# Optimization experiments

Measured on AMD Instinct MI355X. Metric: run time of the kernel, lower is better.

## Reference

```python
import jax, jax.numpy as jnp
import numpy as np

K = 16  # neighbors, incl. self


def setup_inputs() -> dict:
    key = jax.random.key(0)
    ks = jax.random.split(key, 16)
    N, C = 8192, 256  # points, channels (inter_channels == in_channels == C)
    s = 0.05
    inp = {
        'coords': jax.random.uniform(ks[0], (N, 3), dtype=jnp.float32) * 100.0,
        'feats': jax.random.normal(ks[1], (N, C), dtype=jnp.float32),
        'theta_w': jax.random.normal(ks[2], (C, C), dtype=jnp.float32) * s,
        'theta_b': jax.random.normal(ks[3], (C,), dtype=jnp.float32) * s,
        'phi_w': jax.random.normal(ks[4], (C, C), dtype=jnp.float32) * s,
        'phi_b': jax.random.normal(ks[5], (C,), dtype=jnp.float32) * s,
        'g_w': jax.random.normal(ks[6], (C, C), dtype=jnp.float32) * s,
        'g_b': jax.random.normal(ks[7], (C,), dtype=jnp.float32) * s,
        'pe1_w1': jax.random.normal(ks[8], (3, C), dtype=jnp.float32) * s,
        'pe1_b1': jax.random.normal(ks[9], (C,), dtype=jnp.float32) * s,
        'pe1_w2': jax.random.normal(ks[10], (C, C), dtype=jnp.float32) * s,
        'pe1_b2': jax.random.normal(ks[11], (C,), dtype=jnp.float32) * s,
        'W_w': jax.random.normal(ks[12], (C, C), dtype=jnp.float32) * s,
        'W_b': jax.random.normal(ks[13], (C,), dtype=jnp.float32) * s,
    }
    return inp


def reference(coords, feats, theta_w, theta_b, phi_w, phi_b, g_w, g_b,
              pe1_w1, pe1_b1, pe1_w2, pe1_b2, W_w, W_b):
    C = feats.shape[-1]
    # KNN (squared dists, includes self as nearest) == pytorch3d knn_points
    sq = jnp.sum(coords * coords, axis=-1)  # [N]
    d2 = sq[:, None] + sq[None, :] - 2.0 * (coords @ coords.T)  # [N,N]
    _, idx = jax.lax.top_k(-d2, K)  # [N,K] sorted by ascending distance

    nn_coords = coords[idx]            # [N,K,3] knn gather
    nn_feats = feats[idx]              # [N,K,C]

    theta_f = feats @ theta_w + theta_b          # [N,C]
    phi_f = nn_feats @ phi_w + phi_b             # [N,K,C]

    delta_coords = nn_coords - coords[:, None, :]  # [N,K,3]
    # pe1 MLP; NOTE: original code uses pe1 for both pe1 and pe2 (shared)
    pe = jax.nn.relu(delta_coords @ pe1_w1 + pe1_b1) @ pe1_w2 + pe1_b2  # [N,K,C]

    delta_features = (pe * (theta_f[:, None, :] - phi_f) + pe) / jnp.sqrt(jnp.float32(C))
    sim = jax.nn.softmax(delta_features, axis=1)  # softmax over K neighbors

    g_feats = nn_feats @ g_w + g_b               # [N,K,C]
    y = jnp.sum(sim * g_feats, axis=1)           # [N,C]

    # W (1x1 Minkowski conv == per-point linear) + residual
    return y @ W_w + W_b + feats
```

## Files before the change

### kernel.cpp

```cpp
#include <hip/hip_runtime.h>

typedef __bf16 bf16_t;
typedef bf16_t bf16x8 __attribute__((ext_vector_type(8)));
typedef bf16_t bf16x4 __attribute__((ext_vector_type(4)));
typedef bf16_t bf16x2 __attribute__((ext_vector_type(2)));
typedef float f32x4 __attribute__((ext_vector_type(4)));
typedef unsigned long long u64;

#define N_PTS 8192
#define C_DIM 256
#define K_NN 16

#define GRID_G    16
#define GRID_NC   (GRID_G * GRID_G * GRID_G)
#define GRID_CELL 6.25f
#define GRID_INV  0.16f

#define CAST_NBLK 2048
#define PREPW_NBLK 320
__global__ __launch_bounds__(256) void prep_kernel(
    const float* __restrict__ feats, bf16_t* __restrict__ fb,
    const float* __restrict__ w0, const float* __restrict__ w1,
    const float* __restrict__ w2, const float* __restrict__ w3,
    const float* __restrict__ w4, bf16_t* __restrict__ wt_base,
    int* __restrict__ cellCount, int* __restrict__ gcount) {
    const int b = blockIdx.x;
    const int t = threadIdx.x;

    if (b < CAST_NBLK) {
        int i = (b * 256 + t) * 4;
        float4 v = *(const float4*)(feats + i);
        bf16x4 o;
        o[0] = (bf16_t)v.x; o[1] = (bf16_t)v.y; o[2] = (bf16_t)v.z; o[3] = (bf16_t)v.w;
        *(bf16x4*)(fb + i) = o;
    } else if (b < CAST_NBLK + PREPW_NBLK) {
        int pb = b - CAST_NBLK;
        int m = pb >> 6;
        int bx = pb & 63;
        const float* src = (m == 0) ? w0 : (m == 1) ? w1 : (m == 2) ? w2 : (m == 3) ? w3 : w4;
        bf16_t* dst = wt_base + m * (C_DIM * C_DIM);
#pragma unroll
        for (int i = 0; i < 4; ++i) {
            int o = bx * 1024 + i * 256 + t;
            int tkb = o >> 9;
            int rem = o & 511;
            int lm = rem >> 5;
            int r = rem & 31;
            int k = (tkb & 7) * 32 + r;
            int n = (tkb >> 3) * 16 + lm;
            dst[o] = (bf16_t)src[k * C_DIM + n];
        }
    } else {
        int zb = b - CAST_NBLK - PREPW_NBLK;
        cellCount[zb * 256 + t] = 0;
        if (zb == 0 && t == 0) *gcount = 0;
    }
}

__global__ __launch_bounds__(256) void grid_count_kernel(const float* __restrict__ coords,
                                                         int* __restrict__ cellCount,
                                                         int* __restrict__ cid) {
    int i = blockIdx.x * 256 + threadIdx.x;
    float x = coords[3 * i + 0], y = coords[3 * i + 1], z = coords[3 * i + 2];
    int cx = (int)(x * GRID_INV); if (cx > GRID_G - 1) cx = GRID_G - 1;
    int cy = (int)(y * GRID_INV); if (cy > GRID_G - 1) cy = GRID_G - 1;
    int cz = (int)(z * GRID_INV); if (cz > GRID_G - 1) cz = GRID_G - 1;
    int c = (cx * GRID_G + cy) * GRID_G + cz;
    cid[i] = c;
    atomicAdd(&cellCount[c], 1);
}

__global__ __launch_bounds__(256) void grid_scan_kernel(const int* __restrict__ cellCount,
                                                        int* __restrict__ cellStart,
                                                        int* __restrict__ cellPtr) {
    __shared__ int part[256];
    int t = threadIdx.x;
    int base = t * 16;
    int v[16];
    int sum = 0;
#pragma unroll
    for (int i = 0; i < 16; ++i) { v[i] = cellCount[base + i]; sum += v[i]; }
    part[t] = sum;
    __syncthreads();
    for (int off = 1; off < 256; off <<= 1) {
        int x = (t >= off) ? part[t - off] : 0;
        __syncthreads();
        part[t] += x;
        __syncthreads();
    }
    int acc = part[t] - sum;
#pragma unroll
    for (int i = 0; i < 16; ++i) {
        cellStart[base + i] = acc;
        cellPtr[base + i] = acc;
        acc += v[i];
    }
    if (t == 255) cellStart[GRID_NC] = acc;
}

__global__ __launch_bounds__(256) void grid_scatter_kernel(
    const float* __restrict__ coords, const int* __restrict__ cid, int* __restrict__ cellPtr,
    float* __restrict__ sx, float* __restrict__ sy, float* __restrict__ sz,
    float* __restrict__ ssq, int* __restrict__ sidx) {
    int i = blockIdx.x * 256 + threadIdx.x;
    int c = cid[i];
    int pos = atomicAdd(&cellPtr[c], 1);
    float x = coords[3 * i + 0], y = coords[3 * i + 1], z = coords[3 * i + 2];
    sx[pos] = x; sy[pos] = y; sz[pos] = z;
    ssq[pos] = __fadd_rn(__fadd_rn(__fmul_rn(x, x), __fmul_rn(y, y)), __fmul_rn(z, z));
    sidx[pos] = i;
}

__global__ __launch_bounds__(256) void knn_grid_kernel(
    const float* __restrict__ coords, const int* __restrict__ cellStart,
    const float* __restrict__ sx, const float* __restrict__ sy,
    const float* __restrict__ sz, const float* __restrict__ ssq,
    const int* __restrict__ sidx,
    int* __restrict__ idx_out, int* __restrict__ glist, int* __restrict__ gcount) {
    const int tid = threadIdx.x;
    const int wave = tid >> 6, lane = tid & 63;
    const int q = blockIdx.x * 4 + wave;

    __shared__ int segBase[4][25];
    __shared__ int segPref[4][26];

    const float qx = coords[3 * q + 0], qy = coords[3 * q + 1], qz = coords[3 * q + 2];
    const float sqi = __fadd_rn(__fadd_rn(__fmul_rn(qx, qx), __fmul_rn(qy, qy)),
                                __fmul_rn(qz, qz));

    int cx = (int)(qx * GRID_INV); if (cx > GRID_G - 1) cx = GRID_G - 1;
    int cy = (int)(qy * GRID_INV); if (cy > GRID_G - 1) cy = GRID_G - 1;
    int cz = (int)(qz * GRID_INV); if (cz > GRID_G - 1) cz = GRID_G - 1;
    int wx0 = cx - 2; if (wx0 < 0) wx0 = 0;
    int wx1 = cx + 2; if (wx1 > GRID_G - 1) wx1 = GRID_G - 1;
    int wy0 = cy - 2; if (wy0 < 0) wy0 = 0;
    int wy1 = cy + 2; if (wy1 > GRID_G - 1) wy1 = GRID_G - 1;
    int wz0 = cz - 2; if (wz0 < 0) wz0 = 0;
    int wz1 = cz + 2; if (wz1 > GRID_G - 1) wz1 = GRID_G - 1;

    const float INF = __int_as_float(0x7f800000);
    float rc = INF;
    if (wx0 > 0)          rc = fminf(rc, qx - (float)wx0 * GRID_CELL);
    if (wx1 < GRID_G - 1) rc = fminf(rc, (float)(wx1 + 1) * GRID_CELL - qx);
    if (wy0 > 0)          rc = fminf(rc, qy - (float)wy0 * GRID_CELL);
    if (wy1 < GRID_G - 1) rc = fminf(rc, (float)(wy1 + 1) * GRID_CELL - qy);
    if (wz0 > 0)          rc = fminf(rc, qz - (float)wz0 * GRID_CELL);
    if (wz1 < GRID_G - 1) rc = fminf(rc, (float)(wz1 + 1) * GRID_CELL - qz);
    float rc2 = rc * rc * 0.9999f;

    int nx = wx1 - wx0 + 1, nyc = wy1 - wy0 + 1;
    int ns = nx * nyc;
    if (lane < ns) {
        int scx = wx0 + lane / nyc;
        int scy = wy0 + lane % nyc;
        int b = (scx * GRID_G + scy) * GRID_G;
        int s0 = cellStart[b + wz0];
        int s1 = cellStart[b + wz1 + 1];
        segBase[wave][lane] = s0;
        segPref[wave][lane] = s1 - s0;
    }
    __syncthreads();
    if (lane == 0) {
        int acc = 0;
        for (int s = 0; s < ns; ++s) { int l = segPref[wave][s]; segPref[wave][s] = acc; acc += l; }
        segPref[wave][ns] = acc;
    }
    __syncthreads();

    const int M = segPref[wave][ns];
    bool flag = (M < K_NN) || (M > 320);

    u64 k0 = ~0ull, k1 = ~0ull, k2 = ~0ull, k3 = ~0ull, k4 = ~0ull;
    {
        int s = 0;
#pragma unroll
        for (int slot = 0; slot < 5; ++slot) {
            int t = lane + slot * 64;
            if (t < M) {
                while (t >= segPref[wave][s + 1]) ++s;
                int pos = segBase[wave][s] + (t - segPref[wave][s]);
                float x = sx[pos], y = sy[pos], z = sz[pos], sj = ssq[pos];
                float dot = __fmaf_rn(z, qz, __fmaf_rn(y, qy, __fmul_rn(x, qx)));
                float d2 = __fsub_rn(__fadd_rn(sqi, sj), __fmul_rn(2.0f, dot));
                unsigned u = __float_as_uint(d2);
                u = (u & 0x80000000u) ? ~u : (u | 0x80000000u);
                u64 key = (((u64)u) << 32) | (unsigned)sidx[pos];
                if (slot == 0) k0 = key;
                else if (slot == 1) k1 = key;
                else if (slot == 2) k2 = key;
                else if (slot == 3) k3 = key;
                else k4 = key;
            }
        }
    }

    u64 lm2 = k0; int li = 0;
    if (k1 < lm2) { lm2 = k1; li = 1; }
    if (k2 < lm2) { lm2 = k2; li = 2; }
    if (k3 < lm2) { lm2 = k3; li = 3; }
    if (k4 < lm2) { lm2 = k4; li = 4; }
    int keep = 0;
    u64 last = ~0ull;
#pragma unroll 1
    for (int r = 0; r < 16; ++r) {
        u64 w = lm2;
#pragma unroll
        for (int off = 1; off < 64; off <<= 1) {
            u64 o = __shfl_xor(w, off);
            w = (o < w) ? o : w;
        }
        if (lane == r) keep = (int)(unsigned)(w & 0xffffffffull);
        last = w;
        if (lm2 == w) {
            if (li == 0) k0 = ~0ull;
            else if (li == 1) k1 = ~0ull;
            else if (li == 2) k2 = ~0ull;
            else if (li == 3) k3 = ~0ull;
            else k4 = ~0ull;
            lm2 = k0; li = 0;
            if (k1 < lm2) { lm2 = k1; li = 1; }
            if (k2 < lm2) { lm2 = k2; li = 2; }
            if (k3 < lm2) { lm2 = k3; li = 3; }
            if (k4 < lm2) { lm2 = k4; li = 4; }
        }
    }

    if (!flag) {
        unsigned ou = (unsigned)(last >> 32);
        unsigned db = (ou & 0x80000000u) ? (ou ^ 0x80000000u) : ~ou;
        float d16 = __uint_as_float(db);
        if (d16 >= rc2) flag = true;
    }
    if (flag && lane == 0) {
        int sl = atomicAdd(gcount, 1);
        glist[sl] = q;
    }
    if (lane < 16) idx_out[q * K_NN + lane] = keep;
}

__global__ __launch_bounds__(256) void knn_fallback_kernel(const float* __restrict__ coords,
                                                           const int* __restrict__ glist,
                                                           const int* __restrict__ gcount,
                                                           int* __restrict__ idx_out) {
    const int count = *gcount;
    const int n0 = blockIdx.x * 4;
    if (n0 >= count) return;

    const int tid = threadIdx.x;
    const int wave = tid >> 6, lane = tid & 63;
    __shared__ float red16[4][16];
    __shared__ u64 cand[4][256];
    __shared__ int cnt[4];
    __shared__ int qids[4];

    if (tid < 4) {
        cnt[tid] = 0;
        int slot = n0 + tid;
        qids[tid] = glist[slot < count ? slot : count - 1];
    }
    __syncthreads();

    float qx[4], qy[4], qz[4], sqi[4];
#pragma unroll
    for (int q = 0; q < 4; ++q) {
        int id = qids[q];
        qx[q] = coords[3 * id + 0];
        qy[q] = coords[3 * id + 1];
        qz[q] = coords[3 * id + 2];
        sqi[q] = __fadd_rn(__fadd_rn(__fmul_rn(qx[q], qx[q]), __fmul_rn(qy[q], qy[q])),
                           __fmul_rn(qz[q], qz[q]));
    }

    const float INF = __int_as_float(0x7f800000);
    const float* cp = coords + tid * 96;

    float lmin[4] = {INF, INF, INF, INF};
#pragma unroll
    for (int c = 0; c < 4; ++c) {
        float buf[24];
#pragma unroll
        for (int v = 0; v < 6; ++v)
            *(float4*)(buf + v * 4) = *(const float4*)(cp + c * 24 + v * 4);
#pragma unroll
        for (int p = 0; p < 8; ++p) {
            float x = buf[3 * p + 0], y = buf[3 * p + 1], z = buf[3 * p + 2];
            float sqj = __fadd_rn(__fadd_rn(__fmul_rn(x, x), __fmul_rn(y, y)),
                                  __fmul_rn(z, z));
#pragma unroll
            for (int q = 0; q < 4; ++q) {
                float dot = __fmaf_rn(z, qz[q], __fmaf_rn(y, qy[q], __fmul_rn(x, qx[q])));
                float d2 = __fsub_rn(__fadd_rn(sqi[q], sqj), __fmul_rn(2.0f, dot));
                lmin[q] = fminf(lmin[q], d2);
            }
        }
    }

#pragma unroll
    for (int q = 0; q < 4; ++q) {
        float g = lmin[q];
        g = fminf(g, __shfl_xor(g, 1));
        g = fminf(g, __shfl_xor(g, 2));
        g = fminf(g, __shfl_xor(g, 4));
        g = fminf(g, __shfl_xor(g, 8));
        if ((lane & 15) == 0) red16[q][wave * 4 + (lane >> 4)] = g;
    }
    __syncthreads();

    float tau[4];
#pragma unroll
    for (int q = 0; q < 4; ++q) {
        float t = red16[q][0];
#pragma unroll
        for (int i = 1; i < 16; ++i) t = fmaxf(t, red16[q][i]);
        tau[q] = t;
    }

#pragma unroll
    for (int c = 0; c < 4; ++c) {
        float buf[24];
#pragma unroll
        for (int v = 0; v < 6; ++v)
            *(float4*)(buf + v * 4) = *(const float4*)(cp + c * 24 + v * 4);
#pragma unroll
        for (int p = 0; p < 8; ++p) {
            float x = buf[3 * p + 0], y = buf[3 * p + 1], z = buf[3 * p + 2];
            float sqj = __fadd_rn(__fadd_rn(__fmul_rn(x, x), __fmul_rn(y, y)),
                                  __fmul_rn(z, z));
            int j = tid * 32 + c * 8 + p;
#pragma unroll
            for (int q = 0; q < 4; ++q) {
                float dot = __fmaf_rn(z, qz[q], __fmaf_rn(y, qy[q], __fmul_rn(x, qx[q])));
                float d2 = __fsub_rn(__fadd_rn(sqi[q], sqj), __fmul_rn(2.0f, dot));
                if (d2 <= tau[q]) {
                    unsigned u = __float_as_uint(d2);
                    u = (u & 0x80000000u) ? ~u : (u | 0x80000000u);
                    int slot = atomicAdd(&cnt[q], 1);
                    if (slot < 256)
                        cand[q][slot] = (((u64)u) << 32) | (unsigned)j;
                }
            }
        }
    }
    __syncthreads();

    int m = cnt[wave]; if (m > 256) m = 256;
    u64 k0 = ~0ull, k1 = ~0ull, k2 = ~0ull, k3 = ~0ull;
    if (lane < m) k0 = cand[wave][lane];
    if (lane + 64 < m) k1 = cand[wave][lane + 64];
    if (lane + 128 < m) k2 = cand[wave][lane + 128];
    if (lane + 192 < m) k3 = cand[wave][lane + 192];
    u64 lm2 = k0; int li = 0;
    if (k1 < lm2) { lm2 = k1; li = 1; }
    if (k2 < lm2) { lm2 = k2; li = 2; }
    if (k3 < lm2) { lm2 = k3; li = 3; }
    int keep = 0;
#pragma unroll 1
    for (int r = 0; r < 16; ++r) {
        u64 w = lm2;
#pragma unroll
        for (int off = 1; off < 64; off <<= 1) {
            u64 o = __shfl_xor(w, off);
            w = (o < w) ? o : w;
        }
        if (lane == r) keep = (int)(unsigned)(w & 0xffffffffull);
        if (lm2 == w) {
            if (li == 0) k0 = ~0ull;
            else if (li == 1) k1 = ~0ull;
            else if (li == 2) k2 = ~0ull;
            else k3 = ~0ull;
            lm2 = k0; li = 0;
            if (k1 < lm2) { lm2 = k1; li = 1; }
            if (k2 < lm2) { lm2 = k2; li = 2; }
            if (k3 < lm2) { lm2 = k3; li = 3; }
        }
    }
    if (lane < 16) idx_out[qids[wave] * K_NN + lane] = keep;
}

__global__ __launch_bounds__(256, 2) void proj_kernel(
    const bf16_t* __restrict__ fb, const bf16_t* __restrict__ wt_base,
    const float* __restrict__ tb, const float* __restrict__ pb, const float* __restrict__ gb,
    float* __restrict__ T, bf16_t* __restrict__ PG) {
    const int sel = blockIdx.y;
    const int half = blockIdx.z;
    const bf16_t* Wt = wt_base + sel * (C_DIM * C_DIM);
    const float* bias = (sel == 0) ? tb : (sel == 1) ? pb : gb;
    const int wave = threadIdx.x >> 6, lane = threadIdx.x & 63;
    const int q = lane >> 4, lm = lane & 15;
    const int m0 = blockIdx.x * 64;

    bf16x8 bfr[2][8];
#pragma unroll
    for (int ti = 0; ti < 2; ++ti)
#pragma unroll
        for (int kb = 0; kb < 8; ++kb)
            bfr[ti][kb] = *(const bf16x8*)(Wt + (((half * 8 + wave * 2 + ti) * 8 + kb) << 9) + lm * 32 + q * 8);

    float bv[2];
#pragma unroll
    for (int ti = 0; ti < 2; ++ti) bv[ti] = bias[(half * 8 + wave * 2 + ti) * 16 + lm];

#pragma unroll
    for (int p = 0; p < 4; ++p) {
        const bf16_t* arow = fb + (m0 + p * 16 + lm) * C_DIM + q * 8;
        f32x4 acc[2];
        acc[0] = (f32x4){0.f, 0.f, 0.f, 0.f};
        acc[1] = (f32x4){0.f, 0.f, 0.f, 0.f};
#pragma unroll
        for (int kb = 0; kb < 8; ++kb) {
            bf16x8 a = *(const bf16x8*)(arow + kb * 32);
            acc[0] = __builtin_amdgcn_mfma_f32_16x16x32_bf16(a, bfr[0][kb], acc[0], 0, 0, 0);
            acc[1] = __builtin_amdgcn_mfma_f32_16x16x32_bf16(a, bfr[1][kb], acc[1], 0, 0, 0);
        }

#pragma unroll
        for (int ti = 0; ti < 2; ++ti) {
            int c = (half * 8 + wave * 2 + ti) * 16 + lm;
#pragma unroll
            for (int r = 0; r < 4; ++r) {
                float v = acc[ti][r] + bv[ti];
                int off = (m0 + p * 16 + q * 4 + r) * C_DIM + c;
                if (sel == 0) T[off] = v;
                else if (sel == 1) PG[2 * off] = (bf16_t)v;
                else PG[2 * off + 1] = (bf16_t)v;
            }
        }
    }
}

#define HPAD 264
#define P_BLK 8
#define HROWS (P_BLK * 16)
__global__ __launch_bounds__(512, 4) void pe2_fused_kernel(
    const float* __restrict__ coords, const int* __restrict__ idx,
    const float* __restrict__ T, const bf16_t* __restrict__ PG,
    const float* __restrict__ w1, const float* __restrict__ b1, const float* __restrict__ b2,
    const bf16_t* __restrict__ Wt2, bf16_t* __restrict__ yb) {
    __shared__ __align__(16) bf16_t hbuf[2][16 * HPAD];
    __shared__ float dxyz[HROWS][3];
    __shared__ int idxl[HROWS];
    const int tid = threadIdx.x;
    const int p0 = blockIdx.x * P_BLK;
    const int wave = tid >> 6, lane = tid & 63;
    const int q = lane >> 4, lm = lane & 15;

    bf16x8 bfr[2][8];
#pragma unroll
    for (int ti = 0; ti < 2; ++ti)
#pragma unroll
        for (int kb = 0; kb < 8; ++kb)
            bfr[ti][kb] = *(const bf16x8*)(Wt2 + (((wave * 2 + ti) * 8 + kb) << 9) + lm * 32 + q * 8);
    float b2c[2];
#pragma unroll
    for (int ti = 0; ti < 2; ++ti) b2c[ti] = b2[(wave * 2 + ti) * 16 + lm];

    if (tid < HROWS) {
        int n = p0 + (tid >> 4);
        int j = idx[n * K_NN + (tid & 15)];
        idxl[tid] = j;
        dxyz[tid][0] = coords[3 * j + 0] - coords[3 * n + 0];
        dxyz[tid][1] = coords[3 * j + 1] - coords[3 * n + 1];
        dxyz[tid][2] = coords[3 * j + 2] - coords[3 * n + 2];
    }
    __syncthreads();

    const int hc = tid & 255;
    const int rh = (tid >> 8) * 8;
    const float wx = w1[hc], wy = w1[C_DIM + hc], wz = w1[2 * C_DIM + hc], bb = b1[hc];

#pragma unroll
    for (int r = 0; r < 8; ++r) {
        int row = rh + r;
        float pre = dxyz[row][0] * wx + dxyz[row][1] * wy + dxyz[row][2] * wz + bb;
        hbuf[0][row * HPAD + hc] = (bf16_t)fmaxf(pre, 0.0f);
    }
    __syncthreads();

#pragma unroll 1
    for (int lp = 0; lp < P_BLK; ++lp) {
        const int n = p0 + lp;
        const int cur = lp & 1;

        int jr[4];
#pragma unroll
        for (int r = 0; r < 4; ++r) jr[r] = idxl[lp * 16 + q * 4 + r];
        bf16x2 pg[2][4];
        float Tn[2];
#pragma unroll
        for (int ti = 0; ti < 2; ++ti) {
            int c = (wave * 2 + ti) * 16 + lm;
            Tn[ti] = T[n * C_DIM + c];
#pragma unroll
            for (int r = 0; r < 4; ++r)
                pg[ti][r] = *(const bf16x2*)(PG + 2 * (jr[r] * C_DIM + c));
        }

        if (lp + 1 < P_BLK) {
            int rb = (lp + 1) * 16;
#pragma unroll
            for (int r = 0; r < 8; ++r) {
                int row = rh + r;
                float pre = dxyz[rb + row][0] * wx + dxyz[rb + row][1] * wy
                          + dxyz[rb + row][2] * wz + bb;
                hbuf[cur ^ 1][row * HPAD + hc] = (bf16_t)fmaxf(pre, 0.0f);
            }
        }

        const bf16_t* hrow = &hbuf[cur][lm * HPAD + q * 8];
        f32x4 acc[2];
        acc[0] = (f32x4){0.f, 0.f, 0.f, 0.f};
        acc[1] = (f32x4){0.f, 0.f, 0.f, 0.f};
#pragma unroll
        for (int kb = 0; kb < 8; ++kb) {
            bf16x8 a = *(const bf16x8*)(hrow + kb * 32);
            acc[0] = __builtin_amdgcn_mfma_f32_16x16x32_bf16(a, bfr[0][kb], acc[0], 0, 0, 0);
            acc[1] = __builtin_amdgcn_mfma_f32_16x16x32_bf16(a, bfr[1][kb], acc[1], 0, 0, 0);
        }

#pragma unroll
        for (int ti = 0; ti < 2; ++ti) {
            int c = (wave * 2 + ti) * 16 + lm;
            float df[4];
#pragma unroll
            for (int r = 0; r < 4; ++r) {
                float pe = acc[ti][r] + b2c[ti];
                df[r] = (pe * (Tn[ti] - (float)pg[ti][r][0]) + pe) * 0.0625f;
            }
            float mx = fmaxf(fmaxf(df[0], df[1]), fmaxf(df[2], df[3]));
            mx = fmaxf(mx, __shfl_xor(mx, 16));
            mx = fmaxf(mx, __shfl_xor(mx, 32));
            float e[4], s = 0.f;
#pragma unroll
            for (int r = 0; r < 4; ++r) { e[r] = __expf(df[r] - mx); s += e[r]; }
            s += __shfl_xor(s, 16);
            s += __shfl_xor(s, 32);
            float inv = 1.0f / s;
            float y = 0.f;
#pragma unroll
            for (int r = 0; r < 4; ++r) y += e[r] * inv * (float)pg[ti][r][1];
            y += __shfl_xor(y, 16);
            y += __shfl_xor(y, 32);
            if (q == 0) yb[n * C_DIM + c] = (bf16_t)y;
        }
        __syncthreads();
    }
}

__global__ __launch_bounds__(256, 2) void final_kernel(
    const bf16_t* __restrict__ yb, const bf16_t* __restrict__ Wt,
    const float* __restrict__ Wb, const float* __restrict__ feats,
    float* __restrict__ out) {
    const int wave = threadIdx.x >> 6, lane = threadIdx.x & 63;
    const int q = lane >> 4, lm = lane & 15;
    const int m0 = blockIdx.x * 64;
    const int half = blockIdx.y;

    bf16x8 bfr[2][8];
#pragma unroll
    for (int ti = 0; ti < 2; ++ti)
#pragma unroll
        for (int kb = 0; kb < 8; ++kb)
            bfr[ti][kb] = *(const bf16x8*)(Wt + (((half * 8 + wave * 2 + ti) * 8 + kb) << 9) + lm * 32 + q * 8);
    float bv[2];
#pragma unroll
    for (int ti = 0; ti < 2; ++ti) bv[ti] = Wb[(half * 8 + wave * 2 + ti) * 16 + lm];

#pragma unroll
    for (int p = 0; p < 4; ++p) {
        const bf16_t* arow = yb + (m0 + p * 16 + lm) * C_DIM + q * 8;
        f32x4 acc[2];
        acc[0] = (f32x4){0.f, 0.f, 0.f, 0.f};
        acc[1] = (f32x4){0.f, 0.f, 0.f, 0.f};
#pragma unroll
        for (int kb = 0; kb < 8; ++kb) {
            bf16x8 a = *(const bf16x8*)(arow + kb * 32);
            acc[0] = __builtin_amdgcn_mfma_f32_16x16x32_bf16(a, bfr[0][kb], acc[0], 0, 0, 0);
            acc[1] = __builtin_amdgcn_mfma_f32_16x16x32_bf16(a, bfr[1][kb], acc[1], 0, 0, 0);
        }

#pragma unroll
        for (int ti = 0; ti < 2; ++ti) {
            int c = (half * 8 + wave * 2 + ti) * 16 + lm;
#pragma unroll
            for (int r = 0; r < 4; ++r) {
                int off = (m0 + p * 16 + q * 4 + r) * C_DIM + c;
                out[off] = acc[ti][r] + bv[ti] + feats[off];
            }
        }
    }
}

extern "C" void kernel_launch(void* const* d_in, const int* in_sizes, int n_in,
                              void* d_out, int out_size, void* d_ws, size_t ws_size,
                              hipStream_t stream) {
    const float* coords = (const float*)d_in[0];
    const float* feats  = (const float*)d_in[1];
    const float* theta_w = (const float*)d_in[2];
    const float* theta_b = (const float*)d_in[3];
    const float* phi_w   = (const float*)d_in[4];
    const float* phi_b   = (const float*)d_in[5];
    const float* g_w     = (const float*)d_in[6];
    const float* g_b     = (const float*)d_in[7];
    const float* pe1_w1  = (const float*)d_in[8];
    const float* pe1_b1  = (const float*)d_in[9];
    const float* pe1_w2  = (const float*)d_in[10];
    const float* pe1_b2  = (const float*)d_in[11];
    const float* W_w     = (const float*)d_in[12];
    const float* W_b     = (const float*)d_in[13];
    float* out = (float*)d_out;

    char* w = (char*)d_ws;
    size_t off = 0;
    int* idx = (int*)(w + off);        off += (size_t)N_PTS * K_NN * 4;
    bf16_t* fb = (bf16_t*)(w + off);   off += (size_t)N_PTS * C_DIM * 2;
    bf16_t* wt = (bf16_t*)(w + off);   off += (size_t)5 * C_DIM * C_DIM * 2;
    float* T = (float*)(w + off);      off += (size_t)N_PTS * C_DIM * 4;
    bf16_t* PG = (bf16_t*)(w + off);   off += (size_t)N_PTS * C_DIM * 4;
    bf16_t* yb = (bf16_t*)(w + off);   off += (size_t)N_PTS * C_DIM * 2;
    int* cid       = (int*)(w + off);  off += (size_t)N_PTS * 4;
    int* cellCount = (int*)(w + off);  off += (size_t)GRID_NC * 4;
    int* cellStart = (int*)(w + off);  off += (size_t)(GRID_NC + 1) * 4;
    int* cellPtr   = (int*)(w + off);  off += (size_t)GRID_NC * 4;
    float* sxp = (float*)(w + off);    off += (size_t)N_PTS * 4;
    float* syp = (float*)(w + off);    off += (size_t)N_PTS * 4;
    float* szp = (float*)(w + off);    off += (size_t)N_PTS * 4;
    float* ssqp = (float*)(w + off);   off += (size_t)N_PTS * 4;
    int* sidxp = (int*)(w + off);      off += (size_t)N_PTS * 4;
    int* glist = (int*)(w + off);      off += (size_t)N_PTS * 4;
    int* gcount = (int*)(w + off);     off += 256;
    (void)ws_size; (void)in_sizes; (void)n_in; (void)out_size;

    prep_kernel<<<CAST_NBLK + PREPW_NBLK + 16, 256, 0, stream>>>(
        feats, fb, theta_w, phi_w, g_w, pe1_w2, W_w, wt, cellCount, gcount);

    grid_count_kernel<<<N_PTS / 256, 256, 0, stream>>>(coords, cellCount, cid);
    grid_scan_kernel<<<1, 256, 0, stream>>>(cellCount, cellStart, cellPtr);
    grid_scatter_kernel<<<N_PTS / 256, 256, 0, stream>>>(coords, cid, cellPtr,
                                                         sxp, syp, szp, ssqp, sidxp);
    knn_grid_kernel<<<N_PTS / 4, 256, 0, stream>>>(coords, cellStart, sxp, syp, szp,
                                                   ssqp, sidxp, idx, glist, gcount);
    knn_fallback_kernel<<<N_PTS / 4, 256, 0, stream>>>(coords, glist, gcount, idx);

    proj_kernel<<<dim3(N_PTS / 64, 3, 2), 256, 0, stream>>>(fb, wt, theta_b, phi_b, g_b, T, PG);
    pe2_fused_kernel<<<N_PTS / P_BLK, 512, 0, stream>>>(coords, idx, T, PG,
                                                        pe1_w1, pe1_b1, pe1_b2,
                                                        wt + 3 * C_DIM * C_DIM, yb);
    final_kernel<<<dim3(N_PTS / 64, 2), 256, 0, stream>>>(yb, wt + 4 * C_DIM * C_DIM,
                                                          W_b, feats, out);
}
```

Baseline: 197.9 us.

## Pack sorted coords as float4, grid-stride KNN fallback, enlarge pe2 point block

New measurement: 195.5 us. About the same (-1.2%).

```diff
diff --git a/kernel.cpp b/kernel.cpp
--- a/kernel.cpp
+++ b/kernel.cpp
@@ -100,22 +100,19 @@
 
 __global__ __launch_bounds__(256) void grid_scatter_kernel(
     const float* __restrict__ coords, const int* __restrict__ cid, int* __restrict__ cellPtr,
-    float* __restrict__ sx, float* __restrict__ sy, float* __restrict__ sz,
-    float* __restrict__ ssq, int* __restrict__ sidx) {
+    float4* __restrict__ sp4, int* __restrict__ sidx) {
     int i = blockIdx.x * 256 + threadIdx.x;
     int c = cid[i];
     int pos = atomicAdd(&cellPtr[c], 1);
     float x = coords[3 * i + 0], y = coords[3 * i + 1], z = coords[3 * i + 2];
-    sx[pos] = x; sy[pos] = y; sz[pos] = z;
-    ssq[pos] = __fadd_rn(__fadd_rn(__fmul_rn(x, x), __fmul_rn(y, y)), __fmul_rn(z, z));
+    float sq = __fadd_rn(__fadd_rn(__fmul_rn(x, x), __fmul_rn(y, y)), __fmul_rn(z, z));
+    sp4[pos] = make_float4(x, y, z, sq);
     sidx[pos] = i;
 }
 
 __global__ __launch_bounds__(256) void knn_grid_kernel(
     const float* __restrict__ coords, const int* __restrict__ cellStart,
-    const float* __restrict__ sx, const float* __restrict__ sy,
-    const float* __restrict__ sz, const float* __restrict__ ssq,
-    const int* __restrict__ sidx,
+    const float4* __restrict__ sp4, const int* __restrict__ sidx,
     int* __restrict__ idx_out, int* __restrict__ glist, int* __restrict__ gcount) {
     const int tid = threadIdx.x;
     const int wave = tid >> 6, lane = tid & 63;
@@ -179,9 +176,9 @@
             if (t < M) {
                 while (t >= segPref[wave][s + 1]) ++s;
                 int pos = segBase[wave][s] + (t - segPref[wave][s]);
-                float x = sx[pos], y = sy[pos], z = sz[pos], sj = ssq[pos];
-                float dot = __fmaf_rn(z, qz, __fmaf_rn(y, qy, __fmul_rn(x, qx)));
-                float d2 = __fsub_rn(__fadd_rn(sqi, sj), __fmul_rn(2.0f, dot));
+                float4 v = sp4[pos];
+                float dot = __fmaf_rn(v.z, qz, __fmaf_rn(v.y, qy, __fmul_rn(v.x, qx)));
+                float d2 = __fsub_rn(__fadd_rn(sqi, v.w), __fmul_rn(2.0f, dot));
                 unsigned u = __float_as_uint(d2);
                 u = (u & 0x80000000u) ? ~u : (u | 0x80000000u);
                 u64 key = (((u64)u) << 32) | (unsigned)sidx[pos];
@@ -243,138 +240,139 @@
                                                            const int* __restrict__ gcount,
                                                            int* __restrict__ idx_out) {
     const int count = *gcount;
-    const int n0 = blockIdx.x * 4;
-    if (n0 >= count) return;
-
     const int tid = threadIdx.x;
     const int wave = tid >> 6, lane = tid & 63;
     __shared__ float red16[4][16];
     __shared__ u64 cand[4][256];
     __shared__ int cnt[4];
     __shared__ int qids[4];
-
-    if (tid < 4) {
-        cnt[tid] = 0;
-        int slot = n0 + tid;
-        qids[tid] = glist[slot < count ? slot : count - 1];
-    }
-    __syncthreads();
-
-    float qx[4], qy[4], qz[4], sqi[4];
-#pragma unroll
-    for (int q = 0; q < 4; ++q) {
-        int id = qids[q];
-        qx[q] = coords[3 * id + 0];
-        qy[q] = coords[3 * id + 1];
-        qz[q] = coords[3 * id + 2];
-        sqi[q] = __fadd_rn(__fadd_rn(__fmul_rn(qx[q], qx[q]), __fmul_rn(qy[q], qy[q])),
-                           __fmul_rn(qz[q], qz[q]));
-    }
-
     const float INF = __int_as_float(0x7f800000);
     const float* cp = coords + tid * 96;
 
-    float lmin[4] = {INF, INF, INF, INF};
-#pragma unroll
-    for (int c = 0; c < 4; ++c) {
-        float buf[24];
-#pragma unroll
-        for (int v = 0; v < 6; ++v)
-            *(float4*)(buf + v * 4) = *(const float4*)(cp + c * 24 + v * 4);
-#pragma unroll
-        for (int p = 0; p < 8; ++p) {
-            float x = buf[3 * p + 0], y = buf[3 * p + 1], z = buf[3 * p + 2];
-            float sqj = __fadd_rn(__fadd_rn(__fmul_rn(x, x), __fmul_rn(y, y)),
-                                  __fmul_rn(z, z));
-#pragma unroll
-            for (int q = 0; q < 4; ++q) {
-                float dot = __fmaf_rn(z, qz[q], __fmaf_rn(y, qy[q], __fmul_rn(x, qx[q])));
-                float d2 = __fsub_rn(__fadd_rn(sqi[q], sqj), __fmul_rn(2.0f, dot));
-                lmin[q] = fminf(lmin[q], d2);
-            }
-        }
-    }
-
-#pragma unroll
-    for (int q = 0; q < 4; ++q) {
-        float g = lmin[q];
-        g = fminf(g, __shfl_xor(g, 1));
-        g = fminf(g, __shfl_xor(g, 2));
-        g = fminf(g, __shfl_xor(g, 4));
-        g = fminf(g, __shfl_xor(g, 8));
-        if ((lane & 15) == 0) red16[q][wave * 4 + (lane >> 4)] = g;
-    }
-    __syncthreads();
-
-    float tau[4];
-#pragma unroll
-    for (int q = 0; q < 4; ++q) {
-        float t = red16[q][0];
-#pragma unroll
-        for (int i = 1; i < 16; ++i) t = fmaxf(t, red16[q][i]);
-        tau[q] = t;
-    }
-
-#pragma unroll
-    for (int c = 0; c < 4; ++c) {
-        float buf[24];
-#pragma unroll
-        for (int v = 0; v < 6; ++v)
-            *(float4*)(buf + v * 4) = *(const float4*)(cp + c * 24 + v * 4);
-#pragma unroll
-        for (int p = 0; p < 8; ++p) {
-            float x = buf[3 * p + 0], y = buf[3 * p + 1], z = buf[3 * p + 2];
-            float sqj = __fadd_rn(__fadd_rn(__fmul_rn(x, x), __fmul_rn(y, y)),
-                                  __fmul_rn(z, z));
-            int j = tid * 32 + c * 8 + p;
-#pragma unroll
-            for (int q = 0; q < 4; ++q) {
-                float dot = __fmaf_rn(z, qz[q], __fmaf_rn(y, qy[q], __fmul_rn(x, qx[q])));
-                float d2 = __fsub_rn(__fadd_rn(sqi[q], sqj), __fmul_rn(2.0f, dot));
-                if (d2 <= tau[q]) {
-                    unsigned u = __float_as_uint(d2);
-                    u = (u & 0x80000000u) ? ~u : (u | 0x80000000u);
-                    int slot = atomicAdd(&cnt[q], 1);
-                    if (slot < 256)
-                        cand[q][slot] = (((u64)u) << 32) | (unsigned)j;
+#pragma unroll 1
+    for (int n0 = blockIdx.x * 4; n0 < count; n0 += gridDim.x * 4) {
+        if (tid < 4) {
+            cnt[tid] = 0;
+            int slot = n0 + tid;
+            qids[tid] = glist[slot < count ? slot : count - 1];
+        }
+        __syncthreads();
+
+        float qx[4], qy[4], qz[4], sqi[4];
+#pragma unroll
+        for (int q = 0; q < 4; ++q) {
+            int id = qids[q];
+            qx[q] = coords[3 * id + 0];
+            qy[q] = coords[3 * id + 1];
+            qz[q] = coords[3 * id + 2];
+            sqi[q] = __fadd_rn(__fadd_rn(__fmul_rn(qx[q], qx[q]), __fmul_rn(qy[q], qy[q])),
+                               __fmul_rn(qz[q], qz[q]));
+        }
+
+        float lmin[4] = {INF, INF, INF, INF};
+#pragma unroll
+        for (int c = 0; c < 4; ++c) {
+            float buf[24];
+#pragma unroll
+            for (int v = 0; v < 6; ++v)
+                *(float4*)(buf + v * 4) = *(const float4*)(cp + c * 24 + v * 4);
+#pragma unroll
+            for (int p = 0; p < 8; ++p) {
+                float x = buf[3 * p + 0], y = buf[3 * p + 1], z = buf[3 * p + 2];
+                float sqj = __fadd_rn(__fadd_rn(__fmul_rn(x, x), __fmul_rn(y, y)),
+                                      __fmul_rn(z, z));
+#pragma unroll
+                for (int q = 0; q < 4; ++q) {
+                    float dot = __fmaf_rn(z, qz[q], __fmaf_rn(y, qy[q], __fmul_rn(x, qx[q])));
+                    float d2 = __fsub_rn(__fadd_rn(sqi[q], sqj), __fmul_rn(2.0f, dot));
+                    lmin[q] = fminf(lmin[q], d2);
                 }
             }
         }
-    }
-    __syncthreads();
-
-    int m = cnt[wave]; if (m > 256) m = 256;
-    u64 k0 = ~0ull, k1 = ~0ull, k2 = ~0ull, k3 = ~0ull;
-    if (lane < m) k0 = cand[wave][lane];
-    if (lane + 64 < m) k1 = cand[wave][lane + 64];
-    if (lane + 128 < m) k2 = cand[wave][lane + 128];
-    if (lane + 192 < m) k3 = cand[wave][lane + 192];
-    u64 lm2 = k0; int li = 0;
-    if (k1 < lm2) { lm2 = k1; li = 1; }
-    if (k2 < lm2) { lm2 = k2; li = 2; }
-    if (k3 < lm2) { lm2 = k3; li = 3; }
-    int keep = 0;
+
+#pragma unroll
+        for (int q = 0; q < 4; ++q) {
+            float g = lmin[q];
+            g = fminf(g, __shfl_xor(g, 1));
+            g = fminf(g, __shfl_xor(g, 2));
+            g = fminf(g, __shfl_xor(g, 4));
+            g = fminf(g, __shfl_xor(g, 8));
+            if ((lane & 15) == 0) red16[q][wave * 4 + (lane >> 4)] = g;
+        }
+        __syncthreads();
+
+        float tau[4];
+#pragma unroll
+        for (int q = 0; q < 4; ++q) {
+            float t = red16[q][0];
+#pragma unroll
+            for (int i = 1; i < 16; ++i) t = fmaxf(t, red16[q][i]);
+            tau[q] = t;
+        }
+
+#pragma unroll
+        for (int c = 0; c < 4; ++c) {
+            float buf[24];
+#pragma unroll
+            for (int v = 0; v < 6; ++v)
+                *(float4*)(buf + v * 4) = *(const float4*)(cp + c * 24 + v * 4);
+#pragma unroll
+            for (int p = 0; p < 8; ++p) {
+                float x = buf[3 * p + 0], y = buf[3 * p + 1], z = buf[3 * p + 2];
+                float sqj = __fadd_rn(__fadd_rn(__fmul_rn(x, x), __fmul_rn(y, y)),
+                                      __fmul_rn(z, z));
+                int j = tid * 32 + c * 8 + p;
+#pragma unroll
+                for (int q = 0; q < 4; ++q) {
+                    float dot = __fmaf_rn(z, qz[q], __fmaf_rn(y, qy[q], __fmul_rn(x, qx[q])));
+                    float d2 = __fsub_rn(__fadd_rn(sqi[q], sqj), __fmul_rn(2.0f, dot));
+                    if (d2 <= tau[q]) {
+                        unsigned u = __float_as_uint(d2);
+                        u = (u & 0x80000000u) ? ~u : (u | 0x80000000u);
+                        int slot = atomicAdd(&cnt[q], 1);
+                        if (slot < 256)
+                            cand[q][slot] = (((u64)u) << 32) | (unsigned)j;
+                    }
+                }
+            }
+        }
+        __syncthreads();
+
+        int m = cnt[wave]; if (m > 256) m = 256;
+        u64 k0 = ~0ull, k1 = ~0ull, k2 = ~0ull, k3 = ~0ull;
+        if (lane < m) k0 = cand[wave][lane];
+        if (lane + 64 < m) k1 = cand[wave][lane + 64];
+        if (lane + 128 < m) k2 = cand[wave][lane + 128];
+        if (lane + 192 < m) k3 = cand[wave][lane + 192];
+        u64 lm2 = k0; int li = 0;
+        if (k1 < lm2) { lm2 = k1; li = 1; }
+        if (k2 < lm2) { lm2 = k2; li = 2; }
+        if (k3 < lm2) { lm2 = k3; li = 3; }
+        int keep = 0;
 #pragma unroll 1
-    for (int r = 0; r < 16; ++r) {
-        u64 w = lm2;
-#pragma unroll
-        for (int off = 1; off < 64; off <<= 1) {
-            u64 o = __shfl_xor(w, off);
-            w = (o < w) ? o : w;
-        }
-        if (lane == r) keep = (int)(unsigned)(w & 0xffffffffull);
-        if (lm2 == w) {
-            if (li == 0) k0 = ~0ull;
-            else if (li == 1) k1 = ~0ull;
-            else if (li == 2) k2 = ~0ull;
-            else k3 = ~0ull;
-            lm2 = k0; li = 0;
-            if (k1 < lm2) { lm2 = k1; li = 1; }
-            if (k2 < lm2) { lm2 = k2; li = 2; }
-            if (k3 < lm2) { lm2 = k3; li = 3; }
-        }
-    }
-    if (lane < 16) idx_out[qids[wave] * K_NN + lane] = keep;
+        for (int r = 0; r < 16; ++r) {
+            u64 w = lm2;
+#pragma unroll
+            for (int off = 1; off < 64; off <<= 1) {
+                u64 o = __shfl_xor(w, off);
+                w = (o < w) ? o : w;
+            }
+            if (lane == r) keep = (int)(unsigned)(w & 0xffffffffull);
+            if (lm2 == w) {
+                if (li == 0) k0 = ~0ull;
+                else if (li == 1) k1 = ~0ull;
+                else if (li == 2) k2 = ~0ull;
+                else k3 = ~0ull;
+                lm2 = k0; li = 0;
+                if (k1 < lm2) { lm2 = k1; li = 1; }
+                if (k2 < lm2) { lm2 = k2; li = 2; }
+                if (k3 < lm2) { lm2 = k3; li = 3; }
+            }
+        }
+        if (n0 + wave < count && lane < 16)
+            idx_out[qids[wave] * K_NN + lane] = keep;
+        __syncthreads();
+    }
 }
 
 __global__ __launch_bounds__(256, 2) void proj_kernel(
@@ -429,7 +427,7 @@
 }
 
 #define HPAD 264
-#define P_BLK 8
+#define P_BLK 16
 #define HROWS (P_BLK * 16)
 __global__ __launch_bounds__(512, 4) void pe2_fused_kernel(
     const float* __restrict__ coords, const int* __restrict__ idx,
@@ -617,15 +615,12 @@
     float* T = (float*)(w + off);      off += (size_t)N_PTS * C_DIM * 4;
     bf16_t* PG = (bf16_t*)(w + off);   off += (size_t)N_PTS * C_DIM * 4;
     bf16_t* yb = (bf16_t*)(w + off);   off += (size_t)N_PTS * C_DIM * 2;
+    float4* sp4 = (float4*)(w + off);  off += (size_t)N_PTS * 16;
+    int* sidxp = (int*)(w + off);      off += (size_t)N_PTS * 4;
     int* cid       = (int*)(w + off);  off += (size_t)N_PTS * 4;
     int* cellCount = (int*)(w + off);  off += (size_t)GRID_NC * 4;
     int* cellStart = (int*)(w + off);  off += (size_t)(GRID_NC + 1) * 4;
     int* cellPtr   = (int*)(w + off);  off += (size_t)GRID_NC * 4;
-    float* sxp = (float*)(w + off);    off += (size_t)N_PTS * 4;
-    float* syp = (float*)(w + off);    off += (size_t)N_PTS * 4;
-    float* szp = (float*)(w + off);    off += (size_t)N_PTS * 4;
-    float* ssqp = (float*)(w + off);   off += (size_t)N_PTS * 4;
-    int* sidxp = (int*)(w + off);      off += (size_t)N_PTS * 4;
     int* glist = (int*)(w + off);      off += (size_t)N_PTS * 4;
     int* gcount = (int*)(w + off);     off += 256;
     (void)ws_size; (void)in_sizes; (void)n_in; (void)out_size;
@@ -635,11 +630,10 @@
 
     grid_count_kernel<<<N_PTS / 256, 256, 0, stream>>>(coords, cellCount, cid);
     grid_scan_kernel<<<1, 256, 0, stream>>>(cellCount, cellStart, cellPtr);
-    grid_scatter_kernel<<<N_PTS / 256, 256, 0, stream>>>(coords, cid, cellPtr,
-                                                         sxp, syp, szp, ssqp, sidxp);
-    knn_grid_kernel<<<N_PTS / 4, 256, 0, stream>>>(coords, cellStart, sxp, syp, szp,
-                                                   ssqp, sidxp, idx, glist, gcount);
-    knn_fallback_kernel<<<N_PTS / 4, 256, 0, stream>>>(coords, glist, gcount, idx);
+    grid_scatter_kernel<<<N_PTS / 256, 256, 0, stream>>>(coords, cid, cellPtr, sp4, sidxp);
+    knn_grid_kernel<<<N_PTS / 4, 256, 0, stream>>>(coords, cellStart, sp4, sidxp,
+                                                   idx, glist, gcount);
+    knn_fallback_kernel<<<32, 256, 0, stream>>>(coords, glist, gcount, idx);
 
     proj_kernel<<<dim3(N_PTS / 64, 3, 2), 256, 0, stream>>>(fb, wt, theta_b, phi_b, g_b, T, PG);
     pe2_fused_kernel<<<N_PTS / P_BLK, 512, 0, stream>>>(coords, idx, T, PG,
```
